# Kernel optimization log

Measured on AMD Instinct MI355X. Metric: run time of the kernel, lower is better.

Reference implementation:

```python
import jax, jax.numpy as jnp
import numpy as np

N, E, F_IN, H, NC, NG = 50000, 800000, 256, 64, 4, 64

def setup_inputs() -> dict:
    key = jax.random.key(0)
    ks = jax.random.split(key, 12)
    inp = {
        'x': jax.random.normal(ks[0], (N, F_IN), dtype=jnp.float32),
        'edge_index': jax.random.randint(ks[1], (2, E), 0, N, dtype=jnp.int64),
        'batch': jnp.sort(jax.random.randint(ks[2], (N,), 0, NG, dtype=jnp.int64)),
        # GCNConv layer 1 and 2 (weight [in,out] + bias), Glorot-ish scale
        'W1': jax.random.normal(ks[3], (F_IN, H), dtype=jnp.float32) / np.sqrt(F_IN),
        'b1': jnp.zeros((H,), dtype=jnp.float32),
        'W2': jax.random.normal(ks[4], (H, H), dtype=jnp.float32) / np.sqrt(H),
        'b2': jnp.zeros((H,), dtype=jnp.float32),
        # MLP head
        'fc1_w': jax.random.normal(ks[5], (H, 128), dtype=jnp.float32) / np.sqrt(H),
        'fc1_b': jnp.zeros((128,), dtype=jnp.float32),
        'fc2_w': jax.random.normal(ks[6], (128, NC), dtype=jnp.float32) / np.sqrt(128),
        'fc2_b': jnp.zeros((NC,), dtype=jnp.float32),
    }
    return inp

def _gcn_conv(x, src, dst, W, b, n_nodes):
    # PyG GCNConv: add self-loops, symmetric norm D^-1/2 (A+I) D^-1/2, then X W + b
    h = x @ W  # [N, out]
    deg = jax.ops.segment_sum(jnp.ones_like(dst, dtype=h.dtype), dst, num_segments=n_nodes)
    dinv = jnp.where(deg > 0, jax.lax.rsqrt(deg), 0.0)
    norm = dinv[src] * dinv[dst]  # [E+N]
    msg = h[src] * norm[:, None]
    out = jax.ops.segment_sum(msg, dst, num_segments=n_nodes)
    return out + b

def reference(x, edge_index, batch, W1, b1, W2, b2, fc1_w, fc1_b, fc2_w, fc2_b):
    n = x.shape[0]
    loops = jnp.arange(n, dtype=edge_index.dtype)
    src = jnp.concatenate([edge_index[0], loops])
    dst = jnp.concatenate([edge_index[1], loops])
    h = jax.nn.relu(_gcn_conv(x, src, dst, W1, b1, n))
    h = jax.nn.relu(_gcn_conv(h, src, dst, W2, b2, n))
    # global_mean_pool over graph ids
    sums = jax.ops.segment_sum(h, batch, num_segments=NG)
    cnts = jax.ops.segment_sum(jnp.ones((n,), h.dtype), batch, num_segments=NG)
    pooled = sums / jnp.maximum(cnts, 1.0)[:, None]  # [NG, H]
    z = jax.nn.relu(pooled @ fc1_w + fc1_b)
    # dropout in eval mode = identity
    return z @ fc2_w + fc2_b  # [NG, NC]
```

## Files before the change

kernel.cpp:

```cpp
#include <hip/hip_runtime.h>


#define TPB 256
#define CHUNK_A 4096
#define BCAP 4608

typedef unsigned short bfu;
typedef __attribute__((ext_vector_type(8))) short s16x8;
typedef __attribute__((ext_vector_type(4))) float f32x4;

__device__ __forceinline__ float bf2f(bfu u) {
    union { unsigned u32; float f; } c; c.u32 = ((unsigned)u) << 16; return c.f;
}
__device__ __forceinline__ bfu f2bf(float f) {
    union { float f; unsigned u; } c; c.f = f;
    unsigned r = 0x7FFFu + ((c.u >> 16) & 1u);
    return (bfu)((c.u + r) >> 16);
}
__device__ __forceinline__ float blo(unsigned w) {
    union { unsigned u32; float f; } c; c.u32 = w << 16; return c.f;
}
__device__ __forceinline__ float bhi(unsigned w) {
    union { unsigned u32; float f; } c; c.u32 = w & 0xFFFF0000u; return c.f;
}


__global__ __launch_bounds__(TPB) void k_passA(const int* __restrict__ srcv,
                                               const int* __restrict__ dstv, int E,
                                               int* __restrict__ gcur,
                                               int* __restrict__ staged, int nbuck) {
    __shared__ int pk[CHUNK_A];
    __shared__ int hist[256];
    __shared__ int ebase[256];
    __shared__ int gbase[256];
    __shared__ int lcur[256];
    int t = threadIdx.x;
    int e0 = blockIdx.x * CHUNK_A;
    int e1 = e0 + CHUNK_A; if (e1 > E) e1 = E;

    hist[t] = 0; lcur[t] = 0;
    __syncthreads();
    for (int i = e0 + t; i < e1; i += TPB) atomicAdd(&hist[dstv[i] >> 8], 1);
    __syncthreads();
    int v = hist[t];
    ebase[t] = v;
    __syncthreads();
    for (int off = 1; off < 256; off <<= 1) {
        int u = (t >= off) ? ebase[t - off] : 0;
        __syncthreads();
        ebase[t] += u;
        __syncthreads();
    }
    ebase[t] -= v;
    if (t < nbuck && v > 0) gbase[t] = t * BCAP + atomicAdd(&gcur[t], v);
    __syncthreads();
    for (int i = e0 + t; i < e1; i += TPB) {
        int d = dstv[i];
        int s = srcv[i];
        int b = d >> 8;
        int r = atomicAdd(&lcur[b], 1);
        pk[ebase[b] + r] = (s << 8) | (d & 255);
    }
    __syncthreads();
    int wave = t >> 6, lane = t & 63;
    for (int b = wave; b < nbuck; b += 4) {
        int c = hist[b];
        int lb = ebase[b];
        int gb = gbase[b];
        for (int j = lane; j < c; j += 64) staged[gb + j] = pk[lb + j];
    }
}


__global__ __launch_bounds__(TPB) void k_passB(const int* __restrict__ staged,
                                               const int* __restrict__ gcur,
                                               int* __restrict__ csr_off,
                                               int* __restrict__ csr_src,
                                               float* __restrict__ dinv,
                                               int n, int nbuck) {
    __shared__ int pk[BCAP];
    __shared__ int soff[256];
    __shared__ int hist[256];
    __shared__ int nbase[256];
    __shared__ int cur[256];
    int b = blockIdx.x;
    int n0 = b << 8;
    int n1 = n0 + 256; if (n1 > n) n1 = n;
    int cnt = gcur[b];
    int t = threadIdx.x;

    int cv = (t < nbuck) ? gcur[t] : 0;
    soff[t] = cv;
    hist[t] = 0; cur[t] = 0;
    __syncthreads();
    for (int off = 1; off < 256; off <<= 1) {
        int u = (t >= off) ? soff[t - off] : 0;
        __syncthreads();
        soff[t] += u;
        __syncthreads();
    }
    int base = soff[b] - cnt;

    for (int i = t; i < cnt; i += TPB) pk[i] = staged[b * BCAP + i];
    __syncthreads();
    for (int i = t; i < cnt; i += TPB) atomicAdd(&hist[pk[i] & 255], 1);
    __syncthreads();
    int v = hist[t];
    nbase[t] = v;
    __syncthreads();
    for (int off = 1; off < 256; off <<= 1) {
        int u = (t >= off) ? nbase[t - off] : 0;
        __syncthreads();
        nbase[t] += u;
        __syncthreads();
    }
    nbase[t] -= v;
    if (n0 + t < n1) {
        csr_off[n0 + t] = base + nbase[t];
        dinv[n0 + t] = rsqrtf((float)(v + 1));
    }
    if (b == nbuck - 1 && t == 0) csr_off[n] = base + cnt;
    __syncthreads();
    for (int i = t; i < cnt; i += TPB) {
        int p = pk[i];
        int dloc = p & 255;
        int r = atomicAdd(&cur[dloc], 1);
        csr_src[base + nbase[dloc] + r] = p >> 8;
    }
}


__device__ __forceinline__ int swzW(int c, int k) {
    return c * 256 + (k ^ ((c & 15) << 3));
}

__global__ __launch_bounds__(TPB) void k_gemm1(const float* __restrict__ A,
                                               const float* __restrict__ W,
                                               const float* __restrict__ dinv,
                                               bfu* __restrict__ C, int n) {
    const int K = 256;
    __shared__ __align__(16) ushort Bh[64 * 256];

    const int t = threadIdx.x;
    const int wave = t >> 6, lane = t & 63;
    const int rbase = blockIdx.x * 64;

    {
        int c = t & 63;
        int kg = (t >> 6) << 6;
#pragma unroll
        for (int q = 0; q < 8; q++) {
            int k8 = kg + q * 8;
            ushort4 h0, h1;
#pragma unroll
            for (int j = 0; j < 4; j++) ((bfu*)&h0)[j] = f2bf(W[(size_t)(k8 + j) * 64 + c]);
#pragma unroll
            for (int j = 0; j < 4; j++) ((bfu*)&h1)[j] = f2bf(W[(size_t)(k8 + 4 + j) * 64 + c]);
            *(ushort4*)&Bh[swzW(c, k8)]     = h0;
            *(ushort4*)&Bh[swzW(c, k8) + 4] = h1;
        }
    }
    __syncthreads();

    const int rl = lane & 15;
    const int kg8 = (lane >> 4) << 3;
    int r0 = rbase + wave * 16 + rl;
    const float* arow = A + (size_t)(r0 < n ? r0 : (n - 1)) * K;

    f32x4 acc[4];
#pragma unroll
    for (int j = 0; j < 4; j++) acc[j] = {0.f, 0.f, 0.f, 0.f};

#pragma unroll
    for (int ks = 0; ks < 8; ks++) {
        int k0 = ks * 32 + kg8;
        float4 xa = *(const float4*)(arow + k0);
        float4 xb = *(const float4*)(arow + k0 + 4);
        s16x8 af;
        ((bfu*)&af)[0] = f2bf(xa.x);
        ((bfu*)&af)[1] = f2bf(xa.y);
        ((bfu*)&af)[2] = f2bf(xa.z);
        ((bfu*)&af)[3] = f2bf(xa.w);
        ((bfu*)&af)[4] = f2bf(xb.x);
        ((bfu*)&af)[5] = f2bf(xb.y);
        ((bfu*)&af)[6] = f2bf(xb.z);
        ((bfu*)&af)[7] = f2bf(xb.w);
#pragma unroll
        for (int ct = 0; ct < 4; ct++) {
            s16x8 bf = *(const s16x8*)&Bh[swzW(ct * 16 + rl, k0)];
            acc[ct] = __builtin_amdgcn_mfma_f32_16x16x32_bf16(af, bf, acc[ct], 0, 0, 0);
        }
    }

    const int rq = (lane >> 4) << 2;
#pragma unroll
    for (int reg = 0; reg < 4; reg++) {
        int r = rbase + wave * 16 + rq + reg;
        if (r < n) {
            float d = dinv[r];
#pragma unroll
            for (int ct = 0; ct < 4; ct++) {
                C[(size_t)r * 64 + ct * 16 + rl] = f2bf(acc[ct][reg] * d);
            }
        }
    }
}


__device__ __forceinline__ void acc_u4(float* acc, uint4 q) {
    acc[0] += blo(q.x); acc[1] += bhi(q.x);
    acc[2] += blo(q.y); acc[3] += bhi(q.y);
    acc[4] += blo(q.z); acc[5] += bhi(q.z);
    acc[6] += blo(q.w); acc[7] += bhi(q.w);
}

template <bool FUSE>
__global__ __launch_bounds__(TPB) void k_agg(const bfu* __restrict__ hs,
                                             const int* __restrict__ csr_off,
                                             const int* __restrict__ csr_src,
                                             const float* __restrict__ dinv,
                                             const float* __restrict__ bias,
                                             const float* __restrict__ W2,
                                             bfu* __restrict__ out, int n) {
    __shared__ float rowbuf[4][64];
    int wv = threadIdx.x >> 6;
    int node = blockIdx.x * 4 + wv;
    int lane = threadIdx.x & 63;
    int g = lane >> 3;
    int c = lane & 7;
    if (node >= n) return;
    int p0 = csr_off[node];
    int p1 = csr_off[node + 1];
    int deg = p1 - p0;
    float d = dinv[node];

    uint4 selfv = *(const uint4*)(hs + (size_t)node * 64 + c * 8);

    float acc[8];
#pragma unroll
    for (int j = 0; j < 8; j++) acc[j] = 0.f;

    for (int base = 0; base < deg; base += 16) {
        int rem = deg - base;
        int li0 = p0 + base + g;
        if (rem > 8) {
            int li1 = li0 + 8;
            int idx0 = csr_src[li0];
            int idx1 = csr_src[li1 < p1 ? li1 : p0];
            bool v1 = (8 + g) < rem;
            uint4 q0 = *(const uint4*)(hs + (size_t)idx0 * 64 + c * 8);
            uint4 q1 = *(const uint4*)(hs + (size_t)(v1 ? idx1 : node) * 64 + c * 8);
            if (!v1) q1 = make_uint4(0u, 0u, 0u, 0u);
            acc_u4(acc, q0);
            acc_u4(acc, q1);
        } else {
            bool v0 = g < rem;
            int idx0 = csr_src[li0 < p1 ? li0 : p0];
            uint4 q0 = *(const uint4*)(hs + (size_t)(v0 ? idx0 : node) * 64 + c * 8);
            if (!v0) q0 = make_uint4(0u, 0u, 0u, 0u);
            acc_u4(acc, q0);
        }
    }

#pragma unroll
    for (int j = 0; j < 8; j++) {
        acc[j] += __shfl_xor(acc[j], 8);
        acc[j] += __shfl_xor(acc[j], 16);
        acc[j] += __shfl_xor(acc[j], 32);
    }
    acc_u4(acc, selfv);

    float4 b0 = *(const float4*)&bias[c * 8];
    float4 b1 = *(const float4*)&bias[c * 8 + 4];
    float v[8];
    v[0] = fmaxf(d * acc[0] + b0.x, 0.f);
    v[1] = fmaxf(d * acc[1] + b0.y, 0.f);
    v[2] = fmaxf(d * acc[2] + b0.z, 0.f);
    v[3] = fmaxf(d * acc[3] + b0.w, 0.f);
    v[4] = fmaxf(d * acc[4] + b1.x, 0.f);
    v[5] = fmaxf(d * acc[5] + b1.y, 0.f);
    v[6] = fmaxf(d * acc[6] + b1.z, 0.f);
    v[7] = fmaxf(d * acc[7] + b1.w, 0.f);

    if (!FUSE) {
        if (g == 0) {
            uint4 o;
            o.x = (unsigned)f2bf(v[0]) | ((unsigned)f2bf(v[1]) << 16);
            o.y = (unsigned)f2bf(v[2]) | ((unsigned)f2bf(v[3]) << 16);
            o.z = (unsigned)f2bf(v[4]) | ((unsigned)f2bf(v[5]) << 16);
            o.w = (unsigned)f2bf(v[6]) | ((unsigned)f2bf(v[7]) << 16);
            *(uint4*)(out + (size_t)node * 64 + c * 8) = o;
        }
    } else {
        if (g == 0) {
            *(float4*)&rowbuf[wv][c * 8]     = make_float4(v[0], v[1], v[2], v[3]);
            *(float4*)&rowbuf[wv][c * 8 + 4] = make_float4(v[4], v[5], v[6], v[7]);
        }
        __builtin_amdgcn_wave_barrier();
        float a = 0.f;
#pragma unroll 16
        for (int k = 0; k < 64; k++) a += rowbuf[wv][k] * W2[k * 64 + lane];
        out[(size_t)node * 64 + lane] = f2bf(d * a);
    }
}


__global__ __launch_bounds__(TPB) void k_pool(const bfu* __restrict__ h,
                                              const int* __restrict__ batch, int n,
                                              float* __restrict__ gsum,
                                              int* __restrict__ gcnt) {
    const int CH = 16;
    int wid = blockIdx.x * 4 + (threadIdx.x >> 6);
    int lane = threadIdx.x & 63;
    int i0 = wid * CH;
    if (i0 >= n) return;
    int i1 = i0 + CH; if (i1 > n) i1 = n;
    int g0 = batch[i0];
    int g1 = batch[i1 - 1];
    if (g0 == g1) {
        float acc = 0.f;
#pragma unroll
        for (int i = 0; i < CH; i++) {
            int idx = i0 + i;
            if (idx < i1) acc += bf2f(h[(size_t)idx * 64 + lane]);
        }
        atomicAdd(&gsum[g0 * 64 + lane], acc);
        if (lane == 0) atomicAdd(&gcnt[g0], i1 - i0);
    } else {
        int cur = g0;
        float acc = 0.f;
        int cnt = 0;
        for (int i = i0; i < i1; i++) {
            int g = batch[i];
            if (g != cur) {
                atomicAdd(&gsum[cur * 64 + lane], acc);
                if (lane == 0) atomicAdd(&gcnt[cur], cnt);
                acc = 0.f; cnt = 0; cur = g;
            }
            acc += bf2f(h[(size_t)i * 64 + lane]);
            cnt++;
        }
        atomicAdd(&gsum[cur * 64 + lane], acc);
        if (lane == 0) atomicAdd(&gcnt[cur], cnt);
    }
}


__global__ __launch_bounds__(TPB) void k_head1(const float* __restrict__ gsum,
                                               const int* __restrict__ gcnt,
                                               const float* __restrict__ fc1w,
                                               const float* __restrict__ fc1b,
                                               float* __restrict__ z) {
    int t = threadIdx.x;
    int g = blockIdx.x * 2 + (t >> 7);
    int o = t & 127;
    int c = gcnt[g]; if (c < 1) c = 1;
    float inv = 1.0f / (float)c;
    float a = fc1b[o];
#pragma unroll 16
    for (int j = 0; j < 64; j++) {
        float pj = gsum[g * 64 + j] * inv;
        a += pj * fc1w[j * 128 + o];
    }
    z[g * 128 + o] = fmaxf(a, 0.f);
}


__global__ __launch_bounds__(TPB) void k_head2(const float* __restrict__ z,
                                               const float* __restrict__ fc2w,
                                               const float* __restrict__ fc2b,
                                               float* __restrict__ out) {
    int t = threadIdx.x;
    int g = t >> 2, c = t & 3;
    float a = fc2b[c];
#pragma unroll 16
    for (int o = 0; o < 128; o++) a += z[g * 128 + o] * fc2w[o * 4 + c];
    out[t] = a;
}


extern "C" void kernel_launch(void* const* d_in, const int* in_sizes, int n_in,
                              void* d_out, int out_size, void* d_ws, size_t ws_size,
                              hipStream_t stream) {
    const float* x    = (const float*)d_in[0];
    const int*   ei   = (const int*)d_in[1];
    const int*   batch= (const int*)d_in[2];
    const float* W1   = (const float*)d_in[3];
    const float* b1   = (const float*)d_in[4];
    const float* W2   = (const float*)d_in[5];
    const float* b2   = (const float*)d_in[6];
    const float* fc1w = (const float*)d_in[7];
    const float* fc1b = (const float*)d_in[8];
    const float* fc2w = (const float*)d_in[9];
    const float* fc2b = (const float*)d_in[10];

    const int n = in_sizes[2];
    const int E = in_sizes[1] / 2;
    const int* srcv = ei;
    const int* dstv = ei + E;
    const int nbuck = (n + 255) >> 8;

    char* w = (char*)d_ws;
    int*   gcur   = (int*)w;            w += 256 * 4;
    int*   gcnt   = (int*)w;            w += 64 * 4;
    float* gsum   = (float*)w;          w += 64 * 64 * 4;
    size_t zbytes = (size_t)w - (size_t)d_ws;
    int*   csr_off= (int*)w;            w += (size_t)(n + 1) * 4;
    float* dinv   = (float*)w;          w += (size_t)n * 4;
    int*   csr_src= (int*)w;            w += (size_t)E * 4;
    int*   staged = (int*)w;            w += (size_t)nbuck * BCAP * 4;
    float* zbuf   = (float*)w;          w += 64 * 128 * 4;
    w = (char*)(((size_t)w + 255) & ~(size_t)255);
    bfu* hs = (bfu*)w;                  w += (size_t)n * 64 * 2;
    w = (char*)(((size_t)w + 255) & ~(size_t)255);
    bfu* hb = (bfu*)w;                  w += (size_t)n * 64 * 2;

    hipMemsetAsync(d_ws, 0, zbytes, stream);

    int gA = (E + CHUNK_A - 1) / CHUNK_A;
    k_passA<<<gA, TPB, 0, stream>>>(srcv, dstv, E, gcur, staged, nbuck);
    k_passB<<<nbuck, TPB, 0, stream>>>(staged, gcur, csr_off, csr_src, dinv, n, nbuck);

    int gRows = (n + 63) / 64;
    int gNode = (n + 3) / 4;
    k_gemm1<<<gRows, TPB, 0, stream>>>(x, W1, dinv, hs, n);
    k_agg<true><<<gNode, TPB, 0, stream>>>(hs, csr_off, csr_src, dinv, b1, W2, hb, n);
    k_agg<false><<<gNode, TPB, 0, stream>>>(hb, csr_off, csr_src, dinv, b2, nullptr, hs, n);

    int nwaves16 = (n + 15) / 16;
    k_pool<<<(nwaves16 + 3) / 4, TPB, 0, stream>>>(hs, batch, n, gsum, gcnt);
    k_head1<<<32, TPB, 0, stream>>>(gsum, gcnt, fc1w, fc1b, zbuf);
    k_head2<<<1, TPB, 0, stream>>>(zbuf, fc2w, fc2b, (float*)d_out);
}
```

Baseline: 235.6 us.

## Replace two-pass bucketed CSR build with degree-count, scan, atomic scatter

```diff
diff --git a/kernel.cpp b/kernel.cpp
--- a/kernel.cpp
+++ b/kernel.cpp
@@ -2,8 +2,6 @@
 
 
 #define TPB 256
-#define CHUNK_A 4096
-#define BCAP 4608
 
 typedef unsigned short bfu;
 typedef __attribute__((ext_vector_type(8))) short s16x8;
@@ -25,107 +23,55 @@
 }
 
 
-__global__ __launch_bounds__(TPB) void k_passA(const int* __restrict__ srcv,
-                                               const int* __restrict__ dstv, int E,
-                                               int* __restrict__ gcur,
-                                               int* __restrict__ staged, int nbuck) {
-    __shared__ int pk[CHUNK_A];
-    __shared__ int hist[256];
-    __shared__ int ebase[256];
-    __shared__ int gbase[256];
-    __shared__ int lcur[256];
+__global__ __launch_bounds__(TPB) void k_deg(const int* __restrict__ dstv, int E,
+                                             int* __restrict__ deg) {
+    int i = blockIdx.x * TPB + threadIdx.x;
+    if (i < E) atomicAdd(&deg[dstv[i]], 1);
+}
+
+__global__ __launch_bounds__(1024) void k_scan(const int* __restrict__ deg, int n,
+                                               int* __restrict__ csr_off,
+                                               float* __restrict__ dinv) {
+    __shared__ int part[1024];
     int t = threadIdx.x;
-    int e0 = blockIdx.x * CHUNK_A;
-    int e1 = e0 + CHUNK_A; if (e1 > E) e1 = E;
-
-    hist[t] = 0; lcur[t] = 0;
+    int C = (n + 1023) >> 10;
+    int i0 = t * C;
+    int s = 0;
+    for (int j = 0; j < C; j++) {
+        int i = i0 + j;
+        if (i < n) s += deg[i];
+    }
+    part[t] = s;
     __syncthreads();
-    for (int i = e0 + t; i < e1; i += TPB) atomicAdd(&hist[dstv[i] >> 8], 1);
-    __syncthreads();
-    int v = hist[t];
-    ebase[t] = v;
-    __syncthreads();
-    for (int off = 1; off < 256; off <<= 1) {
-        int u = (t >= off) ? ebase[t - off] : 0;
+    for (int off = 1; off < 1024; off <<= 1) {
+        int u = (t >= off) ? part[t - off] : 0;
         __syncthreads();
-        ebase[t] += u;
+        part[t] += u;
         __syncthreads();
     }
-    ebase[t] -= v;
-    if (t < nbuck && v > 0) gbase[t] = t * BCAP + atomicAdd(&gcur[t], v);
-    __syncthreads();
-    for (int i = e0 + t; i < e1; i += TPB) {
+    int run = part[t] - s;
+    for (int j = 0; j < C; j++) {
+        int i = i0 + j;
+        if (i < n) {
+            int dg = deg[i];
+            csr_off[i] = run;
+            dinv[i] = rsqrtf((float)(dg + 1));
+            run += dg;
+        }
+    }
+    if (t == 1023) csr_off[n] = run;
+}
+
+__global__ __launch_bounds__(TPB) void k_scatter(const int* __restrict__ srcv,
+                                                 const int* __restrict__ dstv, int E,
+                                                 const int* __restrict__ csr_off,
+                                                 int* __restrict__ deg,
+                                                 int* __restrict__ csr_src) {
+    int i = blockIdx.x * TPB + threadIdx.x;
+    if (i < E) {
         int d = dstv[i];
-        int s = srcv[i];
-        int b = d >> 8;
-        int r = atomicAdd(&lcur[b], 1);
-        pk[ebase[b] + r] = (s << 8) | (d & 255);
-    }
-    __syncthreads();
-    int wave = t >> 6, lane = t & 63;
-    for (int b = wave; b < nbuck; b += 4) {
-        int c = hist[b];
-        int lb = ebase[b];
-        int gb = gbase[b];
-        for (int j = lane; j < c; j += 64) staged[gb + j] = pk[lb + j];
-    }
-}
-
-
-__global__ __launch_bounds__(TPB) void k_passB(const int* __restrict__ staged,
-                                               const int* __restrict__ gcur,
-                                               int* __restrict__ csr_off,
-                                               int* __restrict__ csr_src,
-                                               float* __restrict__ dinv,
-                                               int n, int nbuck) {
-    __shared__ int pk[BCAP];
-    __shared__ int soff[256];
-    __shared__ int hist[256];
-    __shared__ int nbase[256];
-    __shared__ int cur[256];
-    int b = blockIdx.x;
-    int n0 = b << 8;
-    int n1 = n0 + 256; if (n1 > n) n1 = n;
-    int cnt = gcur[b];
-    int t = threadIdx.x;
-
-    int cv = (t < nbuck) ? gcur[t] : 0;
-    soff[t] = cv;
-    hist[t] = 0; cur[t] = 0;
-    __syncthreads();
-    for (int off = 1; off < 256; off <<= 1) {
-        int u = (t >= off) ? soff[t - off] : 0;
-        __syncthreads();
-        soff[t] += u;
-        __syncthreads();
-    }
-    int base = soff[b] - cnt;
-
-    for (int i = t; i < cnt; i += TPB) pk[i] = staged[b * BCAP + i];
-    __syncthreads();
-    for (int i = t; i < cnt; i += TPB) atomicAdd(&hist[pk[i] & 255], 1);
-    __syncthreads();
-    int v = hist[t];
-    nbase[t] = v;
-    __syncthreads();
-    for (int off = 1; off < 256; off <<= 1) {
-        int u = (t >= off) ? nbase[t - off] : 0;
-        __syncthreads();
-        nbase[t] += u;
-        __syncthreads();
-    }
-    nbase[t] -= v;
-    if (n0 + t < n1) {
-        csr_off[n0 + t] = base + nbase[t];
-        dinv[n0 + t] = rsqrtf((float)(v + 1));
-    }
-    if (b == nbuck - 1 && t == 0) csr_off[n] = base + cnt;
-    __syncthreads();
-    for (int i = t; i < cnt; i += TPB) {
-        int p = pk[i];
-        int dloc = p & 255;
-        int r = atomicAdd(&cur[dloc], 1);
-        csr_src[base + nbase[dloc] + r] = p >> 8;
+        int r = atomicSub(&deg[d], 1) - 1;
+        csr_src[csr_off[d] + r] = srcv[i];
     }
 }
 
@@ -398,17 +344,15 @@
     const int E = in_sizes[1] / 2;
     const int* srcv = ei;
     const int* dstv = ei + E;
-    const int nbuck = (n + 255) >> 8;
 
     char* w = (char*)d_ws;
-    int*   gcur   = (int*)w;            w += 256 * 4;
+    float* gsum   = (float*)w;          w += 64 * 64 * 4;
     int*   gcnt   = (int*)w;            w += 64 * 4;
-    float* gsum   = (float*)w;          w += 64 * 64 * 4;
+    int*   deg    = (int*)w;            w += (size_t)n * 4;
     size_t zbytes = (size_t)w - (size_t)d_ws;
     int*   csr_off= (int*)w;            w += (size_t)(n + 1) * 4;
     float* dinv   = (float*)w;          w += (size_t)n * 4;
     int*   csr_src= (int*)w;            w += (size_t)E * 4;
-    int*   staged = (int*)w;            w += (size_t)nbuck * BCAP * 4;
     float* zbuf   = (float*)w;          w += 64 * 128 * 4;
     w = (char*)(((size_t)w + 255) & ~(size_t)255);
     bfu* hs = (bfu*)w;                  w += (size_t)n * 64 * 2;
@@ -417,9 +361,10 @@
 
     hipMemsetAsync(d_ws, 0, zbytes, stream);
 
-    int gA = (E + CHUNK_A - 1) / CHUNK_A;
-    k_passA<<<gA, TPB, 0, stream>>>(srcv, dstv, E, gcur, staged, nbuck);
-    k_passB<<<nbuck, TPB, 0, stream>>>(staged, gcur, csr_off, csr_src, dinv, n, nbuck);
+    int gE = (E + TPB - 1) / TPB;
+    k_deg<<<gE, TPB, 0, stream>>>(dstv, E, deg);
+    k_scan<<<1, 1024, 0, stream>>>(deg, n, csr_off, dinv);
+    k_scatter<<<gE, TPB, 0, stream>>>(srcv, dstv, E, csr_off, deg, csr_src);
 
     int gRows = (n + 63) / 64;
     int gNode = (n + 3) / 4;
```

Result: slower. 401.7 us (+70.5%).
